# Performance work log

Hardware: AMD Instinct MI355X
Metric: run time of the kernel (lower is better)

## Reference

```python
import jax, jax.numpy as jnp
import numpy as np

H_DIM = 64
GRID = 8
NS = 2.0  # neighborhood_size
S = 256   # number of sequences (scenes)
P = 64    # pedestrians per sequence
EPS = 1e-5


def setup_inputs() -> dict:
    key = jax.random.key(0)
    k = jax.random.split(key, 6)
    N = S * P
    G = GRID * GRID
    h_states = jax.random.normal(k[0], (1, N, H_DIM), jnp.float32)
    end_pos = jax.random.normal(k[1], (N, 2), jnp.float32)
    starts = (jnp.arange(S, dtype=jnp.int32) * P)
    seq_start_end = jnp.stack([starts, starts + P], axis=1)  # (S, 2)
    # mlp_pool: Linear(G*H_DIM -> H_DIM) + BatchNorm1d + ReLU
    W = jax.random.normal(k[2], (G * H_DIM, H_DIM), jnp.float32) / np.sqrt(G * H_DIM)
    b = jnp.zeros((H_DIM,), jnp.float32)
    gamma = jnp.ones((H_DIM,), jnp.float32)
    beta = jnp.zeros((H_DIM,), jnp.float32)
    return {"h_states": h_states, "seq_start_end": seq_start_end, "end_pos": end_pos,
            "W": W, "b": b, "gamma": gamma, "beta": beta}


def reference(h_states, seq_start_end, end_pos, W, b, gamma, beta):
    nseq = seq_start_end.shape[0]          # S (static)
    N = end_pos.shape[0]
    Hd = h_states.shape[-1]
    nped = N // nseq                       # P (static; equal-length sequences)
    G = GRID * GRID
    half = NS / 2.0

    h = h_states.reshape(N, Hd).reshape(nseq, nped, Hd)     # (S, P, H)
    pos = end_pos.reshape(nseq, nped, 2)                    # (S, P, 2)

    # bounds per center pedestrian i
    tl_x = pos[..., 0] - half   # (S, P)
    tl_y = pos[..., 1] + half
    br_x = pos[..., 0] + half
    br_y = pos[..., 1] - half

    # pairwise: axis 1 = center i, axis 2 = other k
    ox = pos[:, None, :, 0]     # (S, 1, P)
    oy = pos[:, None, :, 1]
    cell_x = jnp.floor((ox - tl_x[:, :, None]) / NS * GRID)
    cell_y = jnp.floor((tl_y[:, :, None] - oy) / NS * GRID)
    grid = cell_x + cell_y * GRID                            # (S, P, P)

    oob = ((ox >= br_x[:, :, None]) | (ox <= tl_x[:, :, None]) |
           (oy >= tl_y[:, :, None]) | (oy <= br_y[:, :, None]))
    diag = jnp.eye(nped, dtype=bool)[None]                   # self excluded (within_bound[0::P+1]=1)
    valid = (~oob) & (~diag)

    grid_i = jnp.clip(grid.astype(jnp.int32), 0, G - 1)      # masked entries don't matter
    seq_off = (jnp.arange(nseq, dtype=jnp.int32)[:, None, None] * nped
               + jnp.arange(nped, dtype=jnp.int32)[None, :, None]) * G
    dummy = nseq * nped * G
    ids = jnp.where(valid, seq_off + grid_i, dummy)          # (S, P, P)

    # data for (s, i, k) is hidden of other k (curr_hidden.repeat(num_ped, 1))
    data = jnp.broadcast_to(h[:, None, :, :], (nseq, nped, nped, Hd)).reshape(-1, Hd)
    pooled = jax.ops.segment_sum(data, ids.reshape(-1), num_segments=dummy + 1)[:-1]
    x = pooled.reshape(N, G * Hd)                            # (N, G*H), row i = concat over grid cells

    # mlp_pool: Linear -> BatchNorm1d (train mode, biased var) -> ReLU
    x = x @ W + b
    mu = jnp.mean(x, axis=0)
    var = jnp.mean((x - mu) ** 2, axis=0)
    x = gamma * (x - mu) / jnp.sqrt(var + EPS) + beta
    return jnp.maximum(x, 0.0)
```

## Files before the change

kernel.cpp:

```cpp
#include <hip/hip_runtime.h>
#include <hip/hip_bf16.h>


#define NSEQ 256
#define NTOT (NSEQ*64)
#define EPSV 1e-5f

typedef __attribute__((ext_vector_type(8))) short short8;
typedef __attribute__((ext_vector_type(4))) float f32x4;
typedef unsigned short ushort_t;

__device__ __forceinline__ ushort_t f2b(float f) {
    __hip_bfloat16 h = __float2bfloat16(f);
    return *reinterpret_cast<ushort_t*>(&h);
}
__device__ __forceinline__ int kperm(int k) {
    return ((k >> 5)*2 + ((k & 7) >> 2))*16 + ((k >> 3) & 3)*4 + (k & 3);
}

__global__ __launch_bounds__(256) void sp_transpose(
    const float* __restrict__ W, short* __restrict__ Wt, float* __restrict__ statbuf)
{
    __shared__ __align__(16) float Tl[64*68];
    const int b = blockIdx.x, tid = threadIdx.x;
    if (b == 0 && tid < 128) statbuf[tid] = 0.0f;
    const float* wg = W + (size_t)b*4096;
    for (int m = 0; m < 4; ++m) {
        int c = m*256 + tid;
        int k = c >> 4, t0 = (c & 15)*4;
        *(f32x4*)(Tl + k*68 + t0) = *(const f32x4*)(wg + k*64 + t0);
    }
    __syncthreads();
    for (int m = 0; m < 2; ++m) {
        int q = m*256 + tid;
        int col = q >> 3, k0 = (q & 7)*8;
        short8 o;
        #pragma unroll
        for (int i2 = 0; i2 < 8; ++i2)
            o[i2] = (short)f2b(Tl[kperm(k0 + i2)*68 + col]);
        *(short8*)(Wt + ((size_t)(b*64 + col)*64 + k0)) = o;
    }
}

#define SM_CM   9216
#define SM_POS  13312
#define SM_XS1  17408
#define SM_RED  34816
#define SM_TOT  36864

__global__ __launch_bounds__(512, 2) void sp_main(
    const float* __restrict__ h, const float* __restrict__ pos,
    const short* __restrict__ Wt, const float* __restrict__ bvec,
    float* __restrict__ X, float* __restrict__ statbuf)
{
    __shared__ __align__(16) char smem[SM_TOT];
    ushort_t*      Ht = (ushort_t*)(smem);
    unsigned char* cm = (unsigned char*)(smem + SM_CM);
    float*         px = (float*)(smem + SM_POS);
    float*         py = px + 64;

    const int b    = blockIdx.x;
    const int base = b * 64;
    const int tid  = threadIdx.x;
    const int lane = tid & 63, w = tid >> 6;
    const int ln15 = lane & 15, ln4 = lane >> 4;
    const int xph  = (b >> 3) & 7;

    if (tid < 64) { px[tid] = pos[(base + tid)*2]; py[tid] = pos[(base + tid)*2 + 1]; }
    for (int m = 0; m < 2; ++m) {
        int c = m*512 + tid;
        int j = c >> 4, t0 = (c & 15)*4;
        f32x4 v = *(const f32x4*)(h + (size_t)(base + j)*64 + t0);
        #pragma unroll
        for (int u = 0; u < 4; ++u) Ht[(t0 + u)*72 + j] = f2b(v[u]);
    }
    __syncthreads();

    for (int m = 0; m < 8; ++m) {
        int p = m*512 + tid;
        int i = p >> 6, j = p & 63;
        unsigned char val = 255;
        if (i != j) {
            float ax = px[i], ay = py[i], ox = px[j], oy = py[j];
            float tlx = ax - 1.0f, tly = ay + 1.0f, brx = ax + 1.0f, bry = ay - 1.0f;
            bool oob = (ox >= brx) | (ox <= tlx) | (oy >= tly) | (oy <= bry);
            if (!oob) {
                int g = (int)(floorf((ox - tlx)*4.0f) + floorf((tly - oy)*4.0f)*8.0f);
                g = g < 0 ? 0 : (g > 63 ? 63 : g);
                val = (unsigned char)g;
            }
        }
        cm[i*64 + j] = val;
    }
    __syncthreads();

    short8 hf2[4][2];
    #pragma unroll
    for (int mt = 0; mt < 4; ++mt)
        #pragma unroll
        for (int kt2 = 0; kt2 < 2; ++kt2)
            hf2[mt][kt2] = *(const short8*)(Ht + (mt*16 + ln15)*72 + kt2*32 + ln4*8);

    unsigned ohw[4][2][2];
    {
        const unsigned w8 = (unsigned)(w * 8);
        #pragma unroll
        for (int rt = 0; rt < 4; ++rt)
            #pragma unroll
            for (int kt = 0; kt < 2; ++kt) {
                const unsigned* cp = (const unsigned*)(cm + (rt*16 + ln15)*64 + kt*32 + ln4*8);
                #pragma unroll
                for (int half = 0; half < 2; ++half) {
                    unsigned cw = cp[half], oh = 0u;
                    #pragma unroll
                    for (int u = 0; u < 4; ++u) {
                        unsigned d = ((cw >> (8*u)) & 255u) - w8;
                        if (d < 8u) oh |= (1u << d) << (8*u);
                    }
                    ohw[rt][kt][half] = oh;
                }
            }
    }

    f32x4 acc[4][4];
    #pragma unroll
    for (int rt = 0; rt < 4; ++rt)
        #pragma unroll
        for (int nt = 0; nt < 4; ++nt) acc[rt][nt] = (f32x4){0.f,0.f,0.f,0.f};

    auto load_cell = [&](short8 (&bw)[2][4], int cidx) {
        const int g = w*8 + ((cidx + xph) & 7);
        const short* wg = Wt + (size_t)g*4096;
        #pragma unroll
        for (int kt = 0; kt < 2; ++kt)
            #pragma unroll
            for (int nt = 0; nt < 4; ++nt)
                bw[kt][nt] = *(const short8*)(wg + (nt*16 + ln15)*64 + kt*32 + ln4*8);
    };
    auto compute_cell = [&](const short8 (&bw)[2][4], int cidx) {
        const int c2 = (cidx + xph) & 7;
        #pragma unroll
        for (int rt = 0; rt < 4; ++rt) {
            short8 sf[2];
            #pragma unroll
            for (int kt = 0; kt < 2; ++kt) {
                unsigned t0 = (ohw[rt][kt][0] >> c2) & 0x01010101u;
                unsigned t1 = (ohw[rt][kt][1] >> c2) & 0x01010101u;
                union { unsigned u[4]; short8 s; } sfu;
                sfu.u[0] = ((t0 & 1u)          | ((t0 << 8) & 0x10000u)) * 0x3F80u;
                sfu.u[1] = (((t0 >> 16) & 1u)  | ((t0 >> 8) & 0x10000u)) * 0x3F80u;
                sfu.u[2] = ((t1 & 1u)          | ((t1 << 8) & 0x10000u)) * 0x3F80u;
                sfu.u[3] = (((t1 >> 16) & 1u)  | ((t1 >> 8) & 0x10000u)) * 0x3F80u;
                sf[kt] = sfu.s;
            }
            f32x4 pt[4];
            #pragma unroll
            for (int mt = 0; mt < 4; ++mt) pt[mt] = (f32x4){0.f,0.f,0.f,0.f};
            #pragma unroll
            for (int kt2 = 0; kt2 < 2; ++kt2)
                #pragma unroll
                for (int mt = 0; mt < 4; ++mt)
                    pt[mt] = __builtin_amdgcn_mfma_f32_16x16x32_bf16(hf2[mt][kt2], sf[kt2], pt[mt], 0, 0, 0);
            #pragma unroll
            for (int kt = 0; kt < 2; ++kt) {
                short8 af;
                #pragma unroll
                for (int r = 0; r < 4; ++r) {
                    af[r]     = (short)f2b(pt[2*kt    ][r]);
                    af[4 + r] = (short)f2b(pt[2*kt + 1][r]);
                }
                #pragma unroll
                for (int nt = 0; nt < 4; ++nt)
                    acc[rt][nt] = __builtin_amdgcn_mfma_f32_16x16x32_bf16(af, bw[kt][nt], acc[rt][nt], 0, 0, 0);
            }
        }
    };

    short8 bwA[2][4], bwB[2][4];
    load_cell(bwA, 0);
    #pragma unroll
    for (int cc = 0; cc < 8; cc += 2) {
        if (cc + 1 < 8) load_cell(bwB, cc + 1);
        compute_cell(bwA, cc);
        if (cc + 2 < 8) load_cell(bwA, cc + 2);
        if (cc + 1 < 8) compute_cell(bwB, cc + 1);
    }
    __syncthreads();

    float* Xs0 = (float*)smem;
    float* Xs1 = (float*)(smem + SM_XS1);
    for (int step = 0; step < 4; ++step) {
        if ((w & 3) == step) {
            float* Xs = (w < 4) ? Xs0 : Xs1;
            #pragma unroll
            for (int rt = 0; rt < 4; ++rt)
                #pragma unroll
                for (int nt = 0; nt < 4; ++nt)
                    #pragma unroll
                    for (int r = 0; r < 4; ++r) {
                        int row = rt*16 + ln4*4 + r;
                        int col = nt*16 + ln15;
                        if (step == 0) Xs[row*68 + col]  = acc[rt][nt][r];
                        else           Xs[row*68 + col] += acc[rt][nt][r];
                    }
        }
        __syncthreads();
    }

    {
        const int row = tid >> 3, c0 = (tid & 7)*8;
        float* xg = X + (size_t)(base + row)*64 + c0;
        #pragma unroll
        for (int q = 0; q < 2; ++q) {
            f32x4 v;
            #pragma unroll
            for (int u = 0; u < 4; ++u) {
                int o = row*68 + c0 + q*4 + u;
                v[u] = Xs0[o] + Xs1[o] + bvec[c0 + q*4 + u];
            }
            *(f32x4*)(xg + q*4) = v;
        }
    }

    {
        float* red1 = (float*)(smem + SM_RED);
        float* red2 = red1 + 256;
        if (tid < 256) {
            int col = tid & 63, rg = tid >> 6;
            float bc = bvec[col], s1 = 0.f, s2 = 0.f;
            for (int ii = 0; ii < 16; ++ii) {
                int o = (rg*16 + ii)*68 + col;
                float xv = Xs0[o] + Xs1[o] + bc;
                s1 += xv; s2 += xv*xv;
            }
            red1[rg*64 + col] = s1;
            red2[rg*64 + col] = s2;
        }
        __syncthreads();
        if (tid < 128) {
            int hs = tid >> 6, c2 = tid & 63;
            const float* r0 = hs ? red2 : red1;
            float v = r0[c2] + r0[64 + c2] + r0[128 + c2] + r0[192 + c2];
            atomicAdd(statbuf + tid, v);
        }
    }
}

__global__ __launch_bounds__(256) void sp_finish(
    float* __restrict__ X, const float* __restrict__ statbuf,
    const float* __restrict__ gamma, const float* __restrict__ beta)
{
    __shared__ float scale[64], shift[64];
    const int b = blockIdx.x, tid = threadIdx.x;

    if (tid < 64) {
        const float inv_n = 1.0f / (float)NTOT;
        float mu  = statbuf[tid]      * inv_n;
        float var = statbuf[64 + tid] * inv_n - mu*mu;
        float sc  = gamma[tid] / sqrtf(var + EPSV);
        scale[tid] = sc;
        shift[tid] = beta[tid] - mu*sc;
    }
    __syncthreads();
    #pragma unroll
    for (int q = 0; q < 4; ++q) {
        size_t idx4 = (size_t)b*1024 + q*256 + tid;
        f32x4 v = ((f32x4*)X)[idx4];
        int c0 = ((int)idx4*4) & 63;
        #pragma unroll
        for (int u = 0; u < 4; ++u)
            v[u] = fmaxf(v[u]*scale[c0 + u] + shift[c0 + u], 0.0f);
        ((f32x4*)X)[idx4] = v;
    }
}

extern "C" void kernel_launch(void* const* d_in, const int* in_sizes, int n_in,
                              void* d_out, int out_size, void* d_ws, size_t ws_size,
                              hipStream_t stream)
{
    const float* h     = (const float*)d_in[0];
    const float* pos   = (const float*)d_in[2];
    const float* W     = (const float*)d_in[3];
    const float* bvec  = (const float*)d_in[4];
    const float* gamma = (const float*)d_in[5];
    const float* beta  = (const float*)d_in[6];

    float* X       = (float*)d_out;
    short* Wt      = (short*)d_ws;
    float* statbuf = (float*)((char*)d_ws + 524288);

    sp_transpose<<<64,   256, 0, stream>>>(W, Wt, statbuf);
    sp_main     <<<NSEQ, 512, 0, stream>>>(h, pos, Wt, bvec, X, statbuf);
    sp_finish   <<<NSEQ, 256, 0, stream>>>(X, statbuf, gamma, beta);
}
```

Measured before the change: 101.0 us.

## Split each sequence across two blocks of 32 center rows

The main kernel now launches two blocks per sequence, each handling 32 of the 64 center pedestrians. This halves per-block registers, accumulators and shared memory so launch bounds allow four blocks per CU, and it fills more CUs on a 256-CM-sized grid. The explicit double-buffered weight prefetch is replaced by a simple per-cell load loop. The cost is that every block reloads the full W slice and recomputes the hidden-state transpose for its sequence, doubling that traffic.

Measured after the change: 118.1 us. 1.17x slower.

```diff
diff --git a/kernel.cpp b/kernel.cpp
--- a/kernel.cpp
+++ b/kernel.cpp
@@ -43,12 +43,12 @@
 }
 
 #define SM_CM   9216
-#define SM_POS  13312
-#define SM_XS1  17408
-#define SM_RED  34816
-#define SM_TOT  36864
-
-__global__ __launch_bounds__(512, 2) void sp_main(
+#define SM_POS  11264
+#define SM_XS1  8704
+#define SM_RED  17408
+#define SM_TOT  19456
+
+__global__ __launch_bounds__(512, 4) void sp_main(
     const float* __restrict__ h, const float* __restrict__ pos,
     const short* __restrict__ Wt, const float* __restrict__ bvec,
     float* __restrict__ X, float* __restrict__ statbuf)
@@ -60,7 +60,9 @@
     float*         py = px + 64;
 
     const int b    = blockIdx.x;
-    const int base = b * 64;
+    const int seq  = b >> 1;
+    const int row0 = (b & 1) * 32;
+    const int base = seq * 64;
     const int tid  = threadIdx.x;
     const int lane = tid & 63, w = tid >> 6;
     const int ln15 = lane & 15, ln4 = lane >> 4;
@@ -76,9 +78,10 @@
     }
     __syncthreads();
 
-    for (int m = 0; m < 8; ++m) {
+    for (int m = 0; m < 4; ++m) {
         int p = m*512 + tid;
-        int i = p >> 6, j = p & 63;
+        int il = p >> 6, j = p & 63;
+        int i  = row0 + il;
         unsigned char val = 255;
         if (i != j) {
             float ax = px[i], ay = py[i], ox = px[j], oy = py[j];
@@ -90,7 +93,7 @@
                 val = (unsigned char)g;
             }
         }
-        cm[i*64 + j] = val;
+        cm[il*64 + j] = val;
     }
     __syncthreads();
 
@@ -101,11 +104,11 @@
         for (int kt2 = 0; kt2 < 2; ++kt2)
             hf2[mt][kt2] = *(const short8*)(Ht + (mt*16 + ln15)*72 + kt2*32 + ln4*8);
 
-    unsigned ohw[4][2][2];
+    unsigned ohw[2][2][2];
     {
         const unsigned w8 = (unsigned)(w * 8);
         #pragma unroll
-        for (int rt = 0; rt < 4; ++rt)
+        for (int rt = 0; rt < 2; ++rt)
             #pragma unroll
             for (int kt = 0; kt < 2; ++kt) {
                 const unsigned* cp = (const unsigned*)(cm + (rt*16 + ln15)*64 + kt*32 + ln4*8);
@@ -122,25 +125,25 @@
             }
     }
 
-    f32x4 acc[4][4];
+    f32x4 acc[2][4];
     #pragma unroll
-    for (int rt = 0; rt < 4; ++rt)
+    for (int rt = 0; rt < 2; ++rt)
         #pragma unroll
         for (int nt = 0; nt < 4; ++nt) acc[rt][nt] = (f32x4){0.f,0.f,0.f,0.f};
 
-    auto load_cell = [&](short8 (&bw)[2][4], int cidx) {
-        const int g = w*8 + ((cidx + xph) & 7);
-        const short* wg = Wt + (size_t)g*4096;
+    for (int cc = 0; cc < 8; ++cc) {
+        const int c2 = (cc + xph) & 7;
+        const int g  = w*8 + c2;
+        const short* wgp = Wt + (size_t)g*4096;
+        short8 bw[2][4];
         #pragma unroll
         for (int kt = 0; kt < 2; ++kt)
             #pragma unroll
             for (int nt = 0; nt < 4; ++nt)
-                bw[kt][nt] = *(const short8*)(wg + (nt*16 + ln15)*64 + kt*32 + ln4*8);
-    };
-    auto compute_cell = [&](const short8 (&bw)[2][4], int cidx) {
-        const int c2 = (cidx + xph) & 7;
-        #pragma unroll
-        for (int rt = 0; rt < 4; ++rt) {
+                bw[kt][nt] = *(const short8*)(wgp + (nt*16 + ln15)*64 + kt*32 + ln4*8);
+
+        #pragma unroll
+        for (int rt = 0; rt < 2; ++rt) {
             short8 sf[2];
             #pragma unroll
             for (int kt = 0; kt < 2; ++kt) {
@@ -174,16 +177,6 @@
                     acc[rt][nt] = __builtin_amdgcn_mfma_f32_16x16x32_bf16(af, bw[kt][nt], acc[rt][nt], 0, 0, 0);
             }
         }
-    };
-
-    short8 bwA[2][4], bwB[2][4];
-    load_cell(bwA, 0);
-    #pragma unroll
-    for (int cc = 0; cc < 8; cc += 2) {
-        if (cc + 1 < 8) load_cell(bwB, cc + 1);
-        compute_cell(bwA, cc);
-        if (cc + 2 < 8) load_cell(bwA, cc + 2);
-        if (cc + 1 < 8) compute_cell(bwB, cc + 1);
     }
     __syncthreads();
 
@@ -193,7 +186,7 @@
         if ((w & 3) == step) {
             float* Xs = (w < 4) ? Xs0 : Xs1;
             #pragma unroll
-            for (int rt = 0; rt < 4; ++rt)
+            for (int rt = 0; rt < 2; ++rt)
                 #pragma unroll
                 for (int nt = 0; nt < 4; ++nt)
                     #pragma unroll
@@ -208,18 +201,15 @@
     }
 
     {
-        const int row = tid >> 3, c0 = (tid & 7)*8;
-        float* xg = X + (size_t)(base + row)*64 + c0;
-        #pragma unroll
-        for (int q = 0; q < 2; ++q) {
-            f32x4 v;
-            #pragma unroll
-            for (int u = 0; u < 4; ++u) {
-                int o = row*68 + c0 + q*4 + u;
-                v[u] = Xs0[o] + Xs1[o] + bvec[c0 + q*4 + u];
-            }
-            *(f32x4*)(xg + q*4) = v;
-        }
+        const int lr = tid >> 4, c0 = (tid & 15)*4;
+        float* xg = X + (size_t)(base + row0 + lr)*64 + c0;
+        f32x4 v;
+        #pragma unroll
+        for (int u = 0; u < 4; ++u) {
+            int o = lr*68 + c0 + u;
+            v[u] = Xs0[o] + Xs1[o] + bvec[c0 + u];
+        }
+        *(f32x4*)xg = v;
     }
 
     {
@@ -228,8 +218,8 @@
         if (tid < 256) {
             int col = tid & 63, rg = tid >> 6;
             float bc = bvec[col], s1 = 0.f, s2 = 0.f;
-            for (int ii = 0; ii < 16; ++ii) {
-                int o = (rg*16 + ii)*68 + col;
+            for (int ii = 0; ii < 8; ++ii) {
+                int o = (rg*8 + ii)*68 + col;
                 float xv = Xs0[o] + Xs1[o] + bc;
                 s1 += xv; s2 += xv*xv;
             }
@@ -289,7 +279,7 @@
     short* Wt      = (short*)d_ws;
     float* statbuf = (float*)((char*)d_ws + 524288);
 
-    sp_transpose<<<64,   256, 0, stream>>>(W, Wt, statbuf);
-    sp_main     <<<NSEQ, 512, 0, stream>>>(h, pos, Wt, bvec, X, statbuf);
-    sp_finish   <<<NSEQ, 256, 0, stream>>>(X, statbuf, gamma, beta);
-}
+    sp_transpose<<<64,      256, 0, stream>>>(W, Wt, statbuf);
+    sp_main     <<<NSEQ*2,  512, 0, stream>>>(h, pos, Wt, bvec, X, statbuf);
+    sp_finish   <<<NSEQ,    256, 0, stream>>>(X, statbuf, gamma, beta);
+}
```
